# Kernel tuning notes

Hardware: AMD Instinct MI355X
Metric: run time of the kernel (lower is better)

Reference implementation:

```python
import jax, jax.numpy as jnp
import numpy as np

B, S = 4, 1024           # sequences, tokens per sequence (prefill)
H, HKV, D = 32, 8, 128   # q heads, kv heads (GQA), head_dim
HID = H * D              # 4096
THETA = 10000.0


def setup_inputs() -> dict:
    key = jax.random.key(0)
    k1, k2, k3 = jax.random.split(key, 3)
    T = B * S
    hidden_states = jax.random.normal(k1, (T, HID), jnp.float32) * 0.02
    w_qkv = jax.random.normal(k2, ((H + 2 * HKV) * D, HID), jnp.float32) * 0.02
    w_dense = jax.random.normal(k3, (HID, HID), jnp.float32) * 0.02
    positions = jnp.tile(jnp.arange(S, dtype=jnp.int32), B)  # per-token position ids
    return {"positions": positions, "hidden_states": hidden_states,
            "w_qkv": w_qkv, "w_dense": w_dense}


def _rope(x, positions):
    # NeoX-style rotary embedding (vLLM rotary_dim == head_dim). x: [T, n_heads, D]
    half = D // 2
    inv_freq = 1.0 / (THETA ** (jnp.arange(half, dtype=jnp.float32) / half))
    freqs = positions.astype(jnp.float32)[:, None] * inv_freq       # [T, half]
    cos = jnp.cos(freqs)[:, None, :]
    sin = jnp.sin(freqs)[:, None, :]
    x1, x2 = x[..., :half], x[..., half:]
    return jnp.concatenate([x1 * cos - x2 * sin, x2 * cos + x1 * sin], axis=-1)


def reference(positions, hidden_states, w_qkv, w_dense):
    T = hidden_states.shape[0]
    scale = 1.0 / np.sqrt(D)
    # fused QKV projection (bias=False in config)
    qkv = hidden_states @ w_qkv.T                                   # [T, (H+2*HKV)*D]
    q, k, v = jnp.split(qkv, [H * D, (H + HKV) * D], axis=-1)
    q = q.reshape(T, H, D)
    k = k.reshape(T, HKV, D)
    v = v.reshape(T, HKV, D)
    # fused RoPE on q and k
    q = _rope(q, positions)
    k = _rope(k, positions)
    # causal GQA attention over each sequence
    G = H // HKV
    q = q.reshape(B, S, HKV, G, D)
    k = k.reshape(B, S, HKV, D)
    v = v.reshape(B, S, HKV, D)
    scores = jnp.einsum('bshgd,bthd->bhgst', q, k) * scale          # [B,HKV,G,S,S]
    causal = jnp.tril(jnp.ones((S, S), dtype=bool))
    scores = jnp.where(causal, scores, jnp.finfo(scores.dtype).min)
    probs = jax.nn.softmax(scores, axis=-1)
    attn = jnp.einsum('bhgst,bthd->bshgd', probs, v)                # [B,S,HKV,G,D]
    attn = attn.reshape(T, HID)
    # output projection (skip_bias_add, bias=False -> output only)
    return attn @ w_dense.T
```

## Files before the change

kernel.cpp:

```cpp
#include <hip/hip_runtime.h>

typedef short bf16x8 __attribute__((ext_vector_type(8)));
typedef float f32x4 __attribute__((ext_vector_type(4)));

__device__ __forceinline__ ushort f2bf(float f) {
  union { float f; unsigned u; } x; x.f = f;
  unsigned r = x.u + 0x7fffu + ((x.u >> 16) & 1u);
  return (ushort)(r >> 16);
}
__device__ __forceinline__ float bf2f(ushort u) {
  union { unsigned u; float f; } x; x.u = ((unsigned)u) << 16; return x.f;
}
__device__ __forceinline__ void load_lds16(const void* g, void* l) {
  __builtin_amdgcn_global_load_lds((const __attribute__((address_space(1))) void*)g,
                                   (__attribute__((address_space(3))) void*)l, 16, 0, 0);
}
typedef __attribute__((address_space(3))) const ushort* lds_cp;
__device__ __forceinline__ bf16x8 dsr16(const ushort* p) {
  bf16x8 r;
  asm volatile("ds_read_b128 %0, %1" : "=v"(r) : "v"((lds_cp)p));
  return r;
}
__device__ __forceinline__ void store_out(float* p, float v) { *p = v; }
__device__ __forceinline__ void store_out(ushort* p, float v) { *p = f2bf(v); }

__global__ __launch_bounds__(256) void cast_kernel(const float* __restrict__ in,
                                                   ushort* __restrict__ out, int n4) {
  int i = blockIdx.x * 256 + threadIdx.x;
  if (i < n4) {
    float4 v = ((const float4*)in)[i];
    ushort4 o;
    o.x = f2bf(v.x); o.y = f2bf(v.y); o.z = f2bf(v.z); o.w = f2bf(v.w);
    ((ushort4*)out)[i] = o;
  }
}

#define PBAR() do { asm volatile("" ::: "memory"); __builtin_amdgcn_s_barrier(); \
                    asm volatile("" ::: "memory"); } while (0)
#define WAITL() do { asm volatile("s_waitcnt lgkmcnt(0)" ::: "memory"); \
                     __builtin_amdgcn_sched_barrier(0); } while (0)

template <typename OutT>
__global__ __launch_bounds__(512) void gemm256(const ushort* __restrict__ A,
                                               const ushort* __restrict__ B,
                                               OutT* __restrict__ C,
                                               int M, int N, int K) {
  __shared__ ushort As[2][256 * 64];
  __shared__ ushort Bs[2][256 * 64];
  const int tid = threadIdx.x;
  const int wave = tid >> 6, lane = tid & 63;
  const int quad = lane >> 4, lx = lane & 15;
  const int wr = wave >> 2, wc = wave & 3;
  const int m0 = blockIdx.y * 256, n0 = blockIdx.x * 256;
  const int NT = K >> 6;
  const int sgrow = lane >> 3;
  const int sgchunk = ((lane & 7) ^ sgrow) * 8;

  f32x4 acc[8][4] = {};
  bf16x8 af[4][2], bfr[4][2];

#define STAGE_A(T, H)                                                         \
  do {                                                                        \
    _Pragma("unroll") for (int i_ = 0; i_ < 2; ++i_) {                        \
      const int rg_ = (H) * 128 + wave * 16 + i_ * 8;                         \
      load_lds16(A + (size_t)(m0 + rg_ + sgrow) * K + (T) * 64 + sgchunk,     \
                 &As[(T) & 1][rg_ * 64]);                                     \
    }                                                                         \
  } while (0)
#define STAGE_B(T, H)                                                         \
  do {                                                                        \
    _Pragma("unroll") for (int i_ = 0; i_ < 2; ++i_) {                        \
      const int rg_ = (H) * 128 + wave * 16 + i_ * 8;                         \
      load_lds16(B + (size_t)(n0 + rg_ + sgrow) * K + (T) * 64 + sgchunk,     \
                 &Bs[(T) & 1][rg_ * 64]);                                     \
    }                                                                         \
  } while (0)
#define READ_A(QM)                                                            \
  _Pragma("unroll") for (int mm = 0; mm < 4; ++mm)                            \
  _Pragma("unroll") for (int s = 0; s < 2; ++s)                               \
    af[mm][s] = dsr16(curA + (wr * 128 + ((QM) * 4 + mm) * 16 + lx) * 64      \
                      + (((s * 4 + quad) ^ (lx & 7)) * 8));
#define READ_B(NLO)                                                           \
  _Pragma("unroll") for (int nn = 0; nn < 2; ++nn)                            \
  _Pragma("unroll") for (int s = 0; s < 2; ++s)                               \
    bfr[(NLO) + nn][s] = dsr16(curB + (wc * 64 + ((NLO) + nn) * 16 + lx) * 64 \
                               + (((s * 4 + quad) ^ (lx & 7)) * 8));
#define MFMA_Q(QM, QN)                                                        \
  __builtin_amdgcn_s_setprio(1);                                              \
  _Pragma("unroll") for (int s = 0; s < 2; ++s)                               \
  _Pragma("unroll") for (int mm = 0; mm < 4; ++mm)                            \
  _Pragma("unroll") for (int nn = 0; nn < 2; ++nn)                            \
    acc[(QM) * 4 + mm][(QN) * 2 + nn] = __builtin_amdgcn_mfma_f32_16x16x32_bf16( \
        af[mm][s], bfr[(QN) * 2 + nn][s], acc[(QM) * 4 + mm][(QN) * 2 + nn], 0, 0, 0); \
  __builtin_amdgcn_s_setprio(0);

  STAGE_A(0, 0); STAGE_A(0, 1); STAGE_B(0, 0); STAGE_B(0, 1);
  if (NT > 1) { STAGE_B(1, 0); STAGE_B(1, 1); }

  for (int t = 0; t < NT; ++t) {
    asm volatile("" ::: "memory");
    if (t == NT - 1) { asm volatile("s_waitcnt vmcnt(0)" ::: "memory"); }
    else             { asm volatile("s_waitcnt vmcnt(4)" ::: "memory"); }
    __builtin_amdgcn_s_barrier();
    asm volatile("" ::: "memory");
    const ushort* curA = As[t & 1];
    const ushort* curB = Bs[t & 1];
    READ_A(0); READ_B(0); READ_B(2);
    if (t + 1 < NT) { STAGE_A(t + 1, 0); STAGE_A(t + 1, 1); }
    WAITL();
    PBAR();
    if (t + 2 < NT) { STAGE_B(t + 2, 0); STAGE_B(t + 2, 1); }
    MFMA_Q(0, 0);
    MFMA_Q(0, 1);
    READ_A(1);
    WAITL();
    MFMA_Q(1, 0);
    MFMA_Q(1, 1);
  }

#pragma unroll
  for (int m = 0; m < 8; ++m)
#pragma unroll
    for (int n = 0; n < 4; ++n)
#pragma unroll
      for (int r = 0; r < 4; ++r) {
        const int row = m0 + wr * 128 + m * 16 + quad * 4 + r;
        const int col = n0 + wc * 64 + n * 16 + lx;
        store_out(C + (size_t)row * N + col, acc[m][n][r]);
      }
#undef STAGE_A
#undef STAGE_B
#undef READ_A
#undef READ_B
#undef MFMA_Q
}

__global__ __launch_bounds__(256) void rope_kernel(const int* __restrict__ pos,
                                                   ushort* __restrict__ qkv) {
  const int rid = blockIdx.x * 4 + (threadIdx.x >> 6);
  const int d = threadIdx.x & 63;
  const int t = rid / 40;
  const int hh = rid - t * 40;
  ushort* p = qkv + (size_t)t * 6144 + (hh < 32 ? hh * 128 : 4096 + (hh - 32) * 128);
  const float inv_freq = powf(10000.0f, -(float)d * (1.0f / 64.0f));
  const float fr = (float)pos[t] * inv_freq;
  float sn, cs;
  sincosf(fr, &sn, &cs);
  const float x1 = bf2f(p[d]);
  const float x2 = bf2f(p[d + 64]);
  p[d] = f2bf(x1 * cs - x2 * sn);
  p[d + 64] = f2bf(x2 * cs + x1 * sn);
}

__global__ __launch_bounds__(256) void attn_fused(const ushort* __restrict__ qkv,
                                                  ushort* __restrict__ outb) {
  const int bid = blockIdx.x;
  const int pair = bid & 7;
  const int h = (bid >> 3) & 31;
  const int b = bid >> 8;
  const int kvh = h >> 2;
  const int tid = threadIdx.x, wave = tid >> 6, lane = tid & 63;
  const int quad = lane >> 4, lx = lane & 15;

  __shared__ ushort Ks[64 * 128];
  __shared__ ushort Vt[128 * 64];
  __shared__ ushort Ps[64 * 64];

  const size_t tb = (size_t)b * 1024;
  const float scale = 0.08838834764831843f;

#pragma unroll
  for (int phase = 0; phase < 2; ++phase) {
    const int qt64 = phase ? (15 - pair) : pair;
    const int qrow0 = qt64 * 64 + wave * 16;

    bf16x8 qf[4];
#pragma unroll
    for (int ks = 0; ks < 4; ++ks)
      qf[ks] = *(const bf16x8*)(qkv + (tb + qrow0 + lx) * 6144 + h * 128 + ks * 32 + quad * 8);

    f32x4 o[8] = {};
    float mst[4], lst[4];
#pragma unroll
    for (int r = 0; r < 4; ++r) { mst[r] = -1e30f; lst[r] = 0.f; }

    const int nkt = qt64 + 1;
    for (int it = 0; it < nkt; ++it) {
      const int kb = it * 64;
      __syncthreads();
#pragma unroll
      for (int i = 0; i < 4; ++i) {
        const int rg = wave * 16 + i * 4;
        const int row = rg + quad;
        load_lds16(qkv + (tb + kb + row) * 6144 + 4096 + kvh * 128 + ((lx ^ (row & 7)) * 8),
                   Ks + rg * 128);
      }
      {
        const ushort* vp = qkv + (tb + kb + lane) * 6144 + 5120 + kvh * 128 + wave * 32;
#pragma unroll
        for (int c = 0; c < 4; ++c) {
          bf16x8 v8 = *(const bf16x8*)(vp + c * 8);
#pragma unroll
          for (int e = 0; e < 8; ++e) {
            const int d = wave * 32 + c * 8 + e;
            Vt[d * 64 + (((lane >> 3) ^ (d & 7)) * 8) + (lane & 7)] = (ushort)v8[e];
          }
        }
      }
      __syncthreads();

      f32x4 s[4] = {};
#pragma unroll
      for (int ks = 0; ks < 4; ++ks) {
        bf16x8 kf[4];
#pragma unroll
        for (int kt = 0; kt < 4; ++kt)
          kf[kt] = *(const bf16x8*)(Ks + (kt * 16 + lx) * 128 + (((ks * 4 + quad) ^ (lx & 7)) * 8));
#pragma unroll
        for (int kt = 0; kt < 4; ++kt)
          s[kt] = __builtin_amdgcn_mfma_f32_16x16x32_bf16(qf[ks], kf[kt], s[kt], 0, 0, 0);
      }

      const bool diag = (kb + 63 > qrow0);
#pragma unroll
      for (int r = 0; r < 4; ++r) {
        const int row = qrow0 + quad * 4 + r;
        float mx = -1e30f;
#pragma unroll
        for (int kt = 0; kt < 4; ++kt) {
          float sv = s[kt][r] * scale;
          if (diag && (kb + kt * 16 + lx > row)) sv = -1e30f;
          s[kt][r] = sv;
          mx = fmaxf(mx, sv);
        }
        mx = fmaxf(mx, __shfl_xor(mx, 1));
        mx = fmaxf(mx, __shfl_xor(mx, 2));
        mx = fmaxf(mx, __shfl_xor(mx, 4));
        mx = fmaxf(mx, __shfl_xor(mx, 8));
        const float mnew = fmaxf(mst[r], mx);
        const float alpha = __expf(mst[r] - mnew);
        mst[r] = mnew;
        float rs = 0.f;
#pragma unroll
        for (int kt = 0; kt < 4; ++kt) {
          const float pv = __expf(s[kt][r] - mnew);
          s[kt][r] = pv;
          rs += pv;
        }
        rs += __shfl_xor(rs, 1); rs += __shfl_xor(rs, 2);
        rs += __shfl_xor(rs, 4); rs += __shfl_xor(rs, 8);
        lst[r] = lst[r] * alpha + rs;
#pragma unroll
        for (int dt = 0; dt < 8; ++dt) o[dt][r] *= alpha;
        const int prow = wave * 16 + quad * 4 + r;
#pragma unroll
        for (int kt = 0; kt < 4; ++kt)
          Ps[prow * 64 + (((kt * 2 + (lx >> 3)) ^ (prow & 7)) * 8) + (lx & 7)] = f2bf(s[kt][r]);
      }
      __syncthreads();

#pragma unroll
      for (int ks2 = 0; ks2 < 2; ++ks2) {
        const int prow = wave * 16 + lx;
        bf16x8 pf = *(const bf16x8*)(Ps + prow * 64 + (((ks2 * 4 + quad) ^ (lx & 7)) * 8));
#pragma unroll
        for (int dt = 0; dt < 8; ++dt) {
          bf16x8 vf = *(const bf16x8*)(Vt + (dt * 16 + lx) * 64 + (((ks2 * 4 + quad) ^ (lx & 7)) * 8));
          o[dt] = __builtin_amdgcn_mfma_f32_16x16x32_bf16(pf, vf, o[dt], 0, 0, 0);
        }
      }
    }

#pragma unroll
    for (int r = 0; r < 4; ++r) {
      const float inv = 1.f / lst[r];
      const int row = qrow0 + quad * 4 + r;
#pragma unroll
      for (int dt = 0; dt < 8; ++dt)
        outb[(tb + row) * 4096 + h * 128 + dt * 16 + lx] = f2bf(o[dt][r] * inv);
    }
  }
}

extern "C" void kernel_launch(void* const* d_in, const int* in_sizes, int n_in,
                              void* d_out, int out_size, void* d_ws, size_t ws_size,
                              hipStream_t stream) {
  const int* positions = (const int*)d_in[0];
  const float* hidden  = (const float*)d_in[1];
  const float* w_qkv   = (const float*)d_in[2];
  const float* w_dense = (const float*)d_in[3];
  float* out = (float*)d_out;

  ushort* hidden_bf = (ushort*)d_ws;
  ushort* wqkv_bf   = hidden_bf + (size_t)16777216;
  ushort* wdense_bf = wqkv_bf   + (size_t)25165824;
  ushort* qkv_bf    = wdense_bf + (size_t)16777216;
  ushort* attn_bf   = qkv_bf    + (size_t)25165824;

  cast_kernel<<<16384, 256, 0, stream>>>(hidden,  hidden_bf, 4194304);
  cast_kernel<<<24576, 256, 0, stream>>>(w_qkv,   wqkv_bf,   6291456);
  cast_kernel<<<16384, 256, 0, stream>>>(w_dense, wdense_bf, 4194304);

  gemm256<ushort><<<dim3(24, 16), 512, 0, stream>>>(hidden_bf, wqkv_bf, qkv_bf, 4096, 6144, 4096);

  rope_kernel<<<40960, 256, 0, stream>>>(positions, qkv_bf);

  attn_fused<<<1024, 256, 0, stream>>>(qkv_bf, attn_bf);

  gemm256<float><<<dim3(16, 16), 512, 0, stream>>>(attn_bf, wdense_bf, out, 4096, 4096, 4096);
}
```

Measured before the change: 761.2 us.

## Interleave LDS fragment reads with MFMAs in GEMM inner loop using partial waits

The GEMM K-loop now splits each 64-wide K tile into two 32-wide halves, with separate A and B fragment register sets for each half. Each group of 16 MFMAs is issued as soon as its operands arrive, tracked with partial lgkmcnt waits, while the next fragments are still loading. The old code waited for all LDS reads to finish before computing. This aims to hide LDS read latency behind matrix math. The cost is a tighter, more fragile schedule that depends on exact lgkmcnt counting, plus possible register pressure from keeping four fragment arrays live.

```diff
diff --git a/kernel.cpp b/kernel.cpp
--- a/kernel.cpp
+++ b/kernel.cpp
@@ -37,8 +37,8 @@
 
 #define PBAR() do { asm volatile("" ::: "memory"); __builtin_amdgcn_s_barrier(); \
                     asm volatile("" ::: "memory"); } while (0)
-#define WAITL() do { asm volatile("s_waitcnt lgkmcnt(0)" ::: "memory"); \
-                     __builtin_amdgcn_sched_barrier(0); } while (0)
+#define WAITK(n) do { asm volatile("s_waitcnt lgkmcnt(" #n ")" ::: "memory"); \
+                      __builtin_amdgcn_sched_barrier(0); } while (0)
 
 template <typename OutT>
 __global__ __launch_bounds__(512) void gemm256(const ushort* __restrict__ A,
@@ -57,7 +57,7 @@
   const int sgchunk = ((lane & 7) ^ sgrow) * 8;
 
   f32x4 acc[8][4] = {};
-  bf16x8 af[4][2], bfr[4][2];
+  bf16x8 afA[4], afB[4], bfA[4], bfB[4];
 
 #define STAGE_A(T, H)                                                         \
   do {                                                                        \
@@ -75,23 +75,20 @@
                  &Bs[(T) & 1][rg_ * 64]);                                     \
     }                                                                         \
   } while (0)
-#define READ_A(QM)                                                            \
+#define READ_AF(dst, QM, S)                                                   \
   _Pragma("unroll") for (int mm = 0; mm < 4; ++mm)                            \
-  _Pragma("unroll") for (int s = 0; s < 2; ++s)                               \
-    af[mm][s] = dsr16(curA + (wr * 128 + ((QM) * 4 + mm) * 16 + lx) * 64      \
-                      + (((s * 4 + quad) ^ (lx & 7)) * 8));
-#define READ_B(NLO)                                                           \
-  _Pragma("unroll") for (int nn = 0; nn < 2; ++nn)                            \
-  _Pragma("unroll") for (int s = 0; s < 2; ++s)                               \
-    bfr[(NLO) + nn][s] = dsr16(curB + (wc * 64 + ((NLO) + nn) * 16 + lx) * 64 \
-                               + (((s * 4 + quad) ^ (lx & 7)) * 8));
-#define MFMA_Q(QM, QN)                                                        \
+    dst[mm] = dsr16(curA + (wr * 128 + ((QM) * 4 + mm) * 16 + lx) * 64        \
+                    + ((((S) * 4 + quad) ^ (lx & 7)) * 8));
+#define READ_BF(dst, S)                                                       \
+  _Pragma("unroll") for (int nn = 0; nn < 4; ++nn)                            \
+    dst[nn] = dsr16(curB + (wc * 64 + nn * 16 + lx) * 64                      \
+                    + ((((S) * 4 + quad) ^ (lx & 7)) * 8));
+#define MFMA16(M0, av, bv)                                                    \
   __builtin_amdgcn_s_setprio(1);                                              \
-  _Pragma("unroll") for (int s = 0; s < 2; ++s)                               \
   _Pragma("unroll") for (int mm = 0; mm < 4; ++mm)                            \
-  _Pragma("unroll") for (int nn = 0; nn < 2; ++nn)                            \
-    acc[(QM) * 4 + mm][(QN) * 2 + nn] = __builtin_amdgcn_mfma_f32_16x16x32_bf16( \
-        af[mm][s], bfr[(QN) * 2 + nn][s], acc[(QM) * 4 + mm][(QN) * 2 + nn], 0, 0, 0); \
+  _Pragma("unroll") for (int nn = 0; nn < 4; ++nn)                            \
+    acc[(M0) + mm][nn] = __builtin_amdgcn_mfma_f32_16x16x32_bf16(             \
+        av[mm], bv[nn], acc[(M0) + mm][nn], 0, 0, 0);                         \
   __builtin_amdgcn_s_setprio(0);
 
   STAGE_A(0, 0); STAGE_A(0, 1); STAGE_B(0, 0); STAGE_B(0, 1);
@@ -105,17 +102,22 @@
     asm volatile("" ::: "memory");
     const ushort* curA = As[t & 1];
     const ushort* curB = Bs[t & 1];
-    READ_A(0); READ_B(0); READ_B(2);
+
+    READ_AF(afA, 0, 0); READ_BF(bfA, 0);
+    READ_AF(afB, 1, 0);
     if (t + 1 < NT) { STAGE_A(t + 1, 0); STAGE_A(t + 1, 1); }
-    WAITL();
+    WAITK(4);
+    MFMA16(0, afA, bfA);
+    READ_AF(afA, 0, 1); READ_BF(bfB, 1);
+    WAITK(8);
+    MFMA16(4, afB, bfA);
+    READ_AF(afB, 1, 1);
+    WAITK(4);
     PBAR();
     if (t + 2 < NT) { STAGE_B(t + 2, 0); STAGE_B(t + 2, 1); }
-    MFMA_Q(0, 0);
-    MFMA_Q(0, 1);
-    READ_A(1);
-    WAITL();
-    MFMA_Q(1, 0);
-    MFMA_Q(1, 1);
+    MFMA16(0, afA, bfB);
+    WAITK(0);
+    MFMA16(4, afB, bfB);
   }
 
 #pragma unroll
@@ -130,9 +132,9 @@
       }
 #undef STAGE_A
 #undef STAGE_B
-#undef READ_A
-#undef READ_B
-#undef MFMA_Q
+#undef READ_AF
+#undef READ_BF
+#undef MFMA16
 }
 
 __global__ __launch_bounds__(256) void rope_kernel(const int* __restrict__ pos,
```

Result: no change. 759.4 us (-0.2%).
